# Optimization experiments

Hardware: AMD Instinct MI355X
Metric: run time of the kernel (lower is better)

The kernel has to match this reference:

```python
import jax, jax.numpy as jnp
import numpy as np

N_NODES = 20000
DIM = 128
N_EDGES = 500000
BATCH = 16384
EPS = 1e-6  # torch.nn.PairwiseDistance default eps


def setup_inputs() -> dict:
    key = jax.random.key(0)
    k = jax.random.split(key, 8)
    edges = jax.random.randint(k[0], (2, N_EDGES), 0, N_NODES, dtype=jnp.int64 if jax.config.jax_enable_x64 else jnp.int32)
    nodes_p_star = jnp.sort(jax.random.randint(k[1], (BATCH,), 0, N_NODES))
    nodes_p = jnp.sort(jax.random.randint(k[2], (BATCH,), 0, N_NODES))
    # learned parameters, init in [-1, 1) as in the torch module
    beta_p = 2.0 * jax.random.uniform(k[3], (N_NODES,), dtype=jnp.float32) - 1.0
    beta_p_star = 2.0 * jax.random.uniform(k[4], (N_NODES,), dtype=jnp.float32) - 1.0
    p = 2.0 * jax.random.uniform(k[5], (N_NODES, DIM), dtype=jnp.float32) - 1.0
    p_star = 2.0 * jax.random.uniform(k[6], (N_NODES, DIM), dtype=jnp.float32) - 1.0
    return {
        "edges": edges,
        "nodes_p_star": nodes_p_star,
        "nodes_p": nodes_p,
        "beta_p": beta_p,
        "beta_p_star": beta_p_star,
        "p": p,
        "p_star": p_star,
    }


def reference(edges, nodes_p_star, nodes_p, beta_p, beta_p_star, p, p_star):
    # ---- link term: sum over observed edges of (beta - dist) ----
    beta_pair = beta_p_star[edges[0]] + beta_p[edges[1]]  # [E]
    diff = p[edges[0]] - p_star[edges[1]]                 # [E, D]
    # torch PairwiseDistance adds eps to the difference before the norm
    z_dist = jnp.sqrt(jnp.sum((diff + EPS) ** 2, axis=-1))
    link_term = jnp.sum(beta_pair - z_dist)

    # ---- non-link term: triu-masked sum of exp(beta - cdist) ----
    bps = beta_p_star[nodes_p_star]   # [Ns]
    bp = beta_p[nodes_p]              # [Np]
    ps = p_star[nodes_p_star]         # [Ns, D]
    pp = p[nodes_p]                   # [Np, D]
    beta_mat = bps[None, :] + bp[:, None]          # [Np, Ns]
    # cdist(ps, pp) -> [Ns, Np] via Gram trick
    sq = (jnp.sum(ps * ps, axis=-1)[:, None]
          + jnp.sum(pp * pp, axis=-1)[None, :]
          - 2.0 * jnp.einsum('nd,md->nm', ps, pp))
    dist_mat = jnp.sqrt(jnp.maximum(sq, 0.0))      # [Ns, Np]
    intensity = jnp.exp(beta_mat.T - dist_mat)     # [Ns, Np]
    non_link = jnp.sum(jnp.triu(intensity, k=1))

    return -(link_term - non_link)
```

## Files before the change

### kernel.cpp

```cpp
#include <hip/hip_runtime.h>
#include <hip/hip_bf16.h>

#define N_NODES 20000
#define DIM 128
#define N_EDGES 500000
#define BATCH 16384
#define EPS 1e-6f
#define L2E 1.4426950408889634f

typedef _Float16 half8 __attribute__((ext_vector_type(8)));
typedef _Float16 half4_t __attribute__((ext_vector_type(4)));
typedef float f32x4 __attribute__((ext_vector_type(4)));

__device__ __forceinline__ float fast_sqrtf(float x) {
#if __has_builtin(__builtin_amdgcn_sqrtf)
    return __builtin_amdgcn_sqrtf(x);
#else
    return sqrtf(x);
#endif
}
__device__ __forceinline__ float fast_exp2f(float x) {
#if __has_builtin(__builtin_amdgcn_exp2f)
    return __builtin_amdgcn_exp2f(x);
#else
    return exp2f(x);
#endif
}

#define NB_TILE 16512
#define NB_LINKB 4128
#define NB_MAIN 20640
#define LINK_EPB 128
#define NB_FIN 128

#define OFF_PGEMM 0
#define OFF_PLINK 66048
#define OFF_FPART 82560
#define OFF_PSH   83072
#define OFF_PPH   4277376
#define OFF_N2S   8471680
#define OFF_N2P   8537216
#define OFF_BPS   8602752
#define OFF_BP    8668288
#define OFF_P16   8733824
#define OFF_PS16  13853824
#define OFF_END   18973824

__global__ __launch_bounds__(256) void prep_kernel(
    const float* __restrict__ p, const float* __restrict__ p_star,
    const float* __restrict__ beta_p, const float* __restrict__ beta_ps,
    const int* __restrict__ nodes_ps, const int* __restrict__ nodes_p,
    _Float16* __restrict__ Ah, float* __restrict__ n2A, float* __restrict__ bA2,
    _Float16* __restrict__ Bh, float* __restrict__ n2B, float* __restrict__ bB2,
    _Float16* __restrict__ p16, _Float16* __restrict__ ps16)
{
    const int bx = blockIdx.x;
    const int g = threadIdx.x & 31;
    const int r8 = threadIdx.x >> 5;
    if (bx < 4096) {
        const bool isA = bx < 2048;
        int row = (isA ? bx : bx - 2048) * 8 + r8;
        int id = isA ? nodes_ps[row] : nodes_p[row];
        const float* src = isA ? p_star : p;
        float4 v = ((const float4*)(src + (size_t)id * DIM))[g];
        half4_t o;
        o[0] = (_Float16)v.x; o[1] = (_Float16)v.y; o[2] = (_Float16)v.z; o[3] = (_Float16)v.w;
        _Float16* dst = isA ? Ah : Bh;
        *(half4_t*)(dst + (size_t)row * DIM + g * 4) = o;
        float nrm = v.x * v.x + v.y * v.y + v.z * v.z + v.w * v.w;
        #pragma unroll
        for (int m = 16; m >= 1; m >>= 1) nrm += __shfl_xor(nrm, m, 32);
        if (g == 0) {
            if (isA) { n2A[row] = nrm; bA2[row] = L2E * beta_ps[id]; }
            else     { n2B[row] = nrm; bB2[row] = L2E * beta_p[id]; }
        }
    } else {
        const bool isP = bx < 6596;
        int row = (isP ? bx - 4096 : bx - 6596) * 8 + r8;
        const float* src = isP ? p : p_star;
        _Float16* dst = isP ? p16 : ps16;
        float4 v = ((const float4*)(src + (size_t)row * DIM))[g];
        half4_t o;
        o[0] = (_Float16)v.x; o[1] = (_Float16)v.y; o[2] = (_Float16)v.z; o[3] = (_Float16)v.w;
        *(half4_t*)(dst + (size_t)row * DIM + g * 4) = o;
    }
}

__global__ __launch_bounds__(256) void main_kernel(
    const _Float16* __restrict__ Ag, const _Float16* __restrict__ Bg,
    const float* __restrict__ n2A, const float* __restrict__ n2B,
    const float* __restrict__ bA2, const float* __restrict__ bB2,
    const int* __restrict__ edges,
    const float* __restrict__ beta_p, const float* __restrict__ beta_ps,
    const _Float16* __restrict__ p16, const _Float16* __restrict__ ps16,
    const float* __restrict__ pf, const float* __restrict__ psf, int use16,
    float* __restrict__ pgemm, float* __restrict__ plink)
{
    const int f = blockIdx.x;
    const int grp5 = f / 5, rem5 = f % 5;
    const int tid = threadIdx.x;

    __shared__ __align__(16) _Float16 As[128][136];
    __shared__ __align__(16) _Float16 Bs[64][136];
    __shared__ float smr[4];

    if (rem5 == 4) {
        float tacc = 0.f;
        if (use16) {
            int g = tid & 15, grp = tid >> 4;
            #pragma unroll
            for (int t = 0; t < 8; ++t) {
                int e = grp5 * LINK_EPB + t * 16 + grp;
                if (e < N_EDGES) {
                    int e0 = edges[e];
                    int e1 = edges[N_EDGES + e];
                    half8 a = *(const half8*)(p16 + (size_t)e0 * DIM + g * 8);
                    half8 b = *(const half8*)(ps16 + (size_t)e1 * DIM + g * 8);
                    float s = 0.f;
                    #pragma unroll
                    for (int k = 0; k < 8; ++k) {
                        float d = (float)a[k] - (float)b[k] + EPS;
                        s = fmaf(d, d, s);
                    }
                    #pragma unroll
                    for (int m = 8; m >= 1; m >>= 1) s += __shfl_xor(s, m, 16);
                    if (g == 0) tacc += (beta_ps[e0] + beta_p[e1]) - fast_sqrtf(s);
                }
            }
        } else {
            int g = tid & 31, grp = tid >> 5;
            #pragma unroll
            for (int t = 0; t < 16; ++t) {
                int e = grp5 * LINK_EPB + t * 8 + grp;
                if (e < N_EDGES) {
                    int e0 = edges[e];
                    int e1 = edges[N_EDGES + e];
                    float4 a = ((const float4*)(pf + (size_t)e0 * DIM))[g];
                    float4 b = ((const float4*)(psf + (size_t)e1 * DIM))[g];
                    float dx = a.x - b.x + EPS, dy = a.y - b.y + EPS;
                    float dz = a.z - b.z + EPS, dw = a.w - b.w + EPS;
                    float s = dx * dx + dy * dy + dz * dz + dw * dw;
                    #pragma unroll
                    for (int m = 16; m >= 1; m >>= 1) s += __shfl_xor(s, m, 32);
                    if (g == 0) tacc += (beta_ps[e0] + beta_p[e1]) - fast_sqrtf(s);
                }
            }
        }
        #pragma unroll
        for (int m = 32; m >= 1; m >>= 1) tacc += __shfl_xor(tacc, m, 64);
        if ((tid & 63) == 0) smr[tid >> 6] = tacc;
        __syncthreads();
        if (tid == 0) plink[grp5] = smr[0] + smr[1] + smr[2] + smr[3];
        return;
    }

    const int t = grp5 * 4 + rem5;
    const int by = t / 258, bx = t % 258;
    int ti, tj;
    const int len = 256 - 2 * by;
    if (bx < len) { ti = by; tj = 2 * by + bx; }
    else          { ti = 127 - by; tj = bx - 2; }
    const int i0 = ti * 128;
    const int j0 = tj * 64;

    const int lane = tid & 63;
    const int w = tid >> 6;
    const int wm = w & 1;
    const int wn = w >> 1;
    const int quad = lane >> 4;
    const int lr = lane & 15;
    const int ilo = i0 + wm * 64;
    const int jlo = j0 + wn * 32;

    float4 n2i[4], bi[4];
    float n2j[2], bj[2];
    #pragma unroll
    for (int mi = 0; mi < 4; ++mi) {
        n2i[mi] = *(const float4*)&n2A[ilo + mi * 16 + quad * 4];
        bi[mi] = *(const float4*)&bA2[ilo + mi * 16 + quad * 4];
    }
    #pragma unroll
    for (int ni = 0; ni < 2; ++ni) {
        n2j[ni] = n2B[jlo + ni * 16 + lr];
        bj[ni] = bB2[jlo + ni * 16 + lr];
    }

    #pragma unroll
    for (int c = tid; c < 2048; c += 256)
        *(uint4*)&As[c >> 4][(c & 15) * 8] =
            *(const uint4*)(Ag + (size_t)(i0 + (c >> 4)) * DIM + (c & 15) * 8);
    #pragma unroll
    for (int c = tid; c < 1024; c += 256)
        *(uint4*)&Bs[c >> 4][(c & 15) * 8] =
            *(const uint4*)(Bg + (size_t)(j0 + (c >> 4)) * DIM + (c & 15) * 8);
    __syncthreads();

    const bool dead = (jlo + 31 <= ilo);
    const bool freew = (jlo > ilo + 63);

    float lsum = 0.f;
    if (!dead) {
        f32x4 acc[4][2] = {};
        #pragma unroll
        for (int ks = 0; ks < 4; ++ks) {
            int koff = ks * 32 + quad * 8;
            half8 af[4], bf[2];
            #pragma unroll
            for (int u = 0; u < 4; ++u) af[u] = *(const half8*)&As[wm * 64 + u * 16 + lr][koff];
            #pragma unroll
            for (int u = 0; u < 2; ++u) bf[u] = *(const half8*)&Bs[wn * 32 + u * 16 + lr][koff];
            #pragma unroll
            for (int mi = 0; mi < 4; ++mi)
                #pragma unroll
                for (int ni = 0; ni < 2; ++ni)
                    acc[mi][ni] = __builtin_amdgcn_mfma_f32_16x16x32_f16(af[mi], bf[ni], acc[mi][ni], 0, 0, 0);
        }

        if (freew) {
            #pragma unroll
            for (int mi = 0; mi < 4; ++mi)
                #pragma unroll
                for (int ni = 0; ni < 2; ++ni) {
                    f32x4 d = acc[mi][ni];
                    #pragma unroll
                    for (int r = 0; r < 4; ++r) {
                        float tt = ((const float*)&n2i[mi])[r] + n2j[ni];
                        float sq = fmaxf(fmaf(d[r], -2.f, tt), 0.f);
                        float dist = fast_sqrtf(sq);
                        float arg = fmaf(dist, -L2E, ((const float*)&bi[mi])[r] + bj[ni]);
                        lsum += fast_exp2f(arg);
                    }
                }
        } else {
            #pragma unroll
            for (int mi = 0; mi < 4; ++mi)
                #pragma unroll
                for (int ni = 0; ni < 2; ++ni) {
                    f32x4 d = acc[mi][ni];
                    #pragma unroll
                    for (int r = 0; r < 4; ++r) {
                        int ig = ilo + mi * 16 + quad * 4 + r;
                        int jg = jlo + ni * 16 + lr;
                        float tt = ((const float*)&n2i[mi])[r] + n2j[ni];
                        float sq = fmaxf(fmaf(d[r], -2.f, tt), 0.f);
                        float dist = fast_sqrtf(sq);
                        float arg = fmaf(dist, -L2E, ((const float*)&bi[mi])[r] + bj[ni]);
                        float ex = fast_exp2f(arg);
                        if (jg > ig) lsum += ex;
                    }
                }
        }
    }

    #pragma unroll
    for (int m = 32; m >= 1; m >>= 1) lsum += __shfl_xor(lsum, m, 64);
    if (lane == 0) smr[w] = lsum;
    __syncthreads();
    if (tid == 0) pgemm[t] = smr[0] + smr[1] + smr[2] + smr[3];
}

__global__ __launch_bounds__(256) void reduce1_kernel(
    const float* __restrict__ pg, const float* __restrict__ pl, float* __restrict__ fpart)
{
    float s = 0.f;
    for (int k = blockIdx.x * 256 + threadIdx.x; k < NB_TILE; k += NB_FIN * 256) s += pg[k];
    for (int k = blockIdx.x * 256 + threadIdx.x; k < NB_LINKB; k += NB_FIN * 256) s -= pl[k];
    #pragma unroll
    for (int m = 32; m >= 1; m >>= 1) s += __shfl_xor(s, m, 64);
    __shared__ float sm[4];
    int w = threadIdx.x >> 6;
    if ((threadIdx.x & 63) == 0) sm[w] = s;
    __syncthreads();
    if (threadIdx.x == 0) fpart[blockIdx.x] = sm[0] + sm[1] + sm[2] + sm[3];
}

__global__ __launch_bounds__(128) void reduce2_kernel(
    const float* __restrict__ fpart, float* __restrict__ out)
{
    float s = fpart[threadIdx.x];
    #pragma unroll
    for (int m = 32; m >= 1; m >>= 1) s += __shfl_xor(s, m, 64);
    __shared__ float sm[2];
    if ((threadIdx.x & 63) == 0) sm[threadIdx.x >> 6] = s;
    __syncthreads();
    if (threadIdx.x == 0) out[0] = sm[0] + sm[1];
}

extern "C" void kernel_launch(void* const* d_in, const int* in_sizes, int n_in,
                              void* d_out, int out_size, void* d_ws, size_t ws_size,
                              hipStream_t stream) {
    const int* edges = (const int*)d_in[0];
    const int* nodes_p_star = (const int*)d_in[1];
    const int* nodes_p = (const int*)d_in[2];
    const float* beta_p = (const float*)d_in[3];
    const float* beta_p_star = (const float*)d_in[4];
    const float* p = (const float*)d_in[5];
    const float* p_star = (const float*)d_in[6];

    char* ws = (char*)d_ws;
    float* pgemm = (float*)(ws + OFF_PGEMM);
    float* plink = (float*)(ws + OFF_PLINK);
    float* fpart = (float*)(ws + OFF_FPART);
    _Float16* psh = (_Float16*)(ws + OFF_PSH);
    _Float16* pph = (_Float16*)(ws + OFF_PPH);
    float* n2s = (float*)(ws + OFF_N2S);
    float* n2p = (float*)(ws + OFF_N2P);
    float* bps2 = (float*)(ws + OFF_BPS);
    float* bp2 = (float*)(ws + OFF_BP);
    _Float16* p16 = (_Float16*)(ws + OFF_P16);
    _Float16* ps16 = (_Float16*)(ws + OFF_PS16);

    const int use16 = (ws_size >= (size_t)OFF_END) ? 1 : 0;

    prep_kernel<<<9096, 256, 0, stream>>>(
        p, p_star, beta_p, beta_p_star, nodes_p_star, nodes_p,
        psh, n2s, bps2, pph, n2p, bp2, p16, ps16);

    main_kernel<<<NB_MAIN, 256, 0, stream>>>(
        psh, pph, n2s, n2p, bps2, bp2,
        edges, beta_p, beta_p_star, p16, ps16, p, p_star, use16,
        pgemm, plink);

    reduce1_kernel<<<NB_FIN, 256, 0, stream>>>(pgemm, plink, fpart);
    reduce2_kernel<<<1, 128, 0, stream>>>(fpart, (float*)d_out);
}
```

Baseline: 237.5 us.

## Use 128x128 triangular tiles with 512 threads and fuse link edges into GEMM blocks

Replaces the 128x64 tiles with 128x128 square tiles over the upper triangle, processed by 512-thread blocks on a 2D grid. Instead of dedicated link blocks, each tile block now gathers 64 edges up front and finishes their distances after the MFMA epilogue, so the gather latency overlaps the GEMM. The two-stage reduction becomes a single 1024-thread reduce kernel. The aim is to cut redundant row loads, block count and launch overhead, at the cost of more LDS per block and heavier per-block work.

```diff
diff --git a/kernel.cpp b/kernel.cpp
--- a/kernel.cpp
+++ b/kernel.cpp
@@ -27,24 +27,18 @@
 #endif
 }
 
-#define NB_TILE 16512
-#define NB_LINKB 4128
-#define NB_MAIN 20640
-#define LINK_EPB 128
-#define NB_FIN 128
+#define NB_TILE 8256
 
 #define OFF_PGEMM 0
-#define OFF_PLINK 66048
-#define OFF_FPART 82560
-#define OFF_PSH   83072
-#define OFF_PPH   4277376
-#define OFF_N2S   8471680
-#define OFF_N2P   8537216
-#define OFF_BPS   8602752
-#define OFF_BP    8668288
-#define OFF_P16   8733824
-#define OFF_PS16  13853824
-#define OFF_END   18973824
+#define OFF_PSH   33280
+#define OFF_PPH   4227584
+#define OFF_N2S   8421888
+#define OFF_N2P   8487424
+#define OFF_BPS   8552960
+#define OFF_BP    8618496
+#define OFF_P16   8684032
+#define OFF_PS16  13804032
+#define OFF_END   18924032
 
 __global__ __launch_bounds__(256) void prep_kernel(
     const float* __restrict__ p, const float* __restrict__ p_star,
@@ -86,7 +80,7 @@
     }
 }
 
-__global__ __launch_bounds__(256) void main_kernel(
+__global__ __launch_bounds__(512, 4) void main_kernel(
     const _Float16* __restrict__ Ag, const _Float16* __restrict__ Bg,
     const float* __restrict__ n2A, const float* __restrict__ n2B,
     const float* __restrict__ bA2, const float* __restrict__ bB2,
@@ -94,148 +88,123 @@
     const float* __restrict__ beta_p, const float* __restrict__ beta_ps,
     const _Float16* __restrict__ p16, const _Float16* __restrict__ ps16,
     const float* __restrict__ pf, const float* __restrict__ psf, int use16,
-    float* __restrict__ pgemm, float* __restrict__ plink)
+    float* __restrict__ pgemm)
 {
-    const int f = blockIdx.x;
-    const int grp5 = f / 5, rem5 = f % 5;
+    const int bx = blockIdx.x, by = blockIdx.y;
+    int ti, tj;
+    const int len = 128 - by;
+    if (bx < len) { ti = by; tj = by + bx; }
+    else          { ti = 127 - by; tj = 127 - (bx - len); }
+    const int i0 = ti * 128, j0 = tj * 128;
+    const int bid = by * 129 + bx;
+    const bool diag = (ti == tj);
+
+    __shared__ __align__(16) _Float16 As[128][136];
+    __shared__ __align__(16) _Float16 Bs[128][136];
+    __shared__ float smr[8];
+
     const int tid = threadIdx.x;
-
-    __shared__ __align__(16) _Float16 As[128][136];
-    __shared__ __align__(16) _Float16 Bs[64][136];
-    __shared__ float smr[4];
-
-    if (rem5 == 4) {
-        float tacc = 0.f;
-        if (use16) {
-            int g = tid & 15, grp = tid >> 4;
-            #pragma unroll
-            for (int t = 0; t < 8; ++t) {
-                int e = grp5 * LINK_EPB + t * 16 + grp;
-                if (e < N_EDGES) {
-                    int e0 = edges[e];
-                    int e1 = edges[N_EDGES + e];
-                    half8 a = *(const half8*)(p16 + (size_t)e0 * DIM + g * 8);
-                    half8 b = *(const half8*)(ps16 + (size_t)e1 * DIM + g * 8);
+    const int lane = tid & 63;
+    const int w = tid >> 6;
+    const int wm = w & 3;
+    const int wn = w >> 2;
+    const int quad = lane >> 4;
+    const int lr = lane & 15;
+
+    float lsum = 0.f;
+    half8 ea[2], eb[2];
+    float ebeta[2] = {0.f, 0.f};
+    bool ev[2];
+    {
+        #pragma unroll
+        for (int t = 0; t < 2; ++t) {
+            int e = bid * 64 + w * 8 + quad * 2 + t;
+            ev[t] = (e < N_EDGES);
+            if (ev[t]) {
+                int e0 = edges[e];
+                int e1 = edges[N_EDGES + e];
+                if (use16) {
+                    ea[t] = *(const half8*)(p16 + (size_t)e0 * DIM + lr * 8);
+                    eb[t] = *(const half8*)(ps16 + (size_t)e1 * DIM + lr * 8);
+                    if (lr == 0) ebeta[t] = beta_ps[e0] + beta_p[e1];
+                } else {
+                    const float* ar = pf + (size_t)e0 * DIM + lr * 8;
+                    const float* br = psf + (size_t)e1 * DIM + lr * 8;
                     float s = 0.f;
                     #pragma unroll
                     for (int k = 0; k < 8; ++k) {
-                        float d = (float)a[k] - (float)b[k] + EPS;
+                        float d = ar[k] - br[k] + EPS;
                         s = fmaf(d, d, s);
                     }
                     #pragma unroll
                     for (int m = 8; m >= 1; m >>= 1) s += __shfl_xor(s, m, 16);
-                    if (g == 0) tacc += (beta_ps[e0] + beta_p[e1]) - fast_sqrtf(s);
+                    if (lr == 0) lsum -= (beta_ps[e0] + beta_p[e1]) - fast_sqrtf(s);
                 }
             }
-        } else {
-            int g = tid & 31, grp = tid >> 5;
-            #pragma unroll
-            for (int t = 0; t < 16; ++t) {
-                int e = grp5 * LINK_EPB + t * 8 + grp;
-                if (e < N_EDGES) {
-                    int e0 = edges[e];
-                    int e1 = edges[N_EDGES + e];
-                    float4 a = ((const float4*)(pf + (size_t)e0 * DIM))[g];
-                    float4 b = ((const float4*)(psf + (size_t)e1 * DIM))[g];
-                    float dx = a.x - b.x + EPS, dy = a.y - b.y + EPS;
-                    float dz = a.z - b.z + EPS, dw = a.w - b.w + EPS;
-                    float s = dx * dx + dy * dy + dz * dz + dw * dw;
-                    #pragma unroll
-                    for (int m = 16; m >= 1; m >>= 1) s += __shfl_xor(s, m, 32);
-                    if (g == 0) tacc += (beta_ps[e0] + beta_p[e1]) - fast_sqrtf(s);
-                }
-            }
-        }
-        #pragma unroll
-        for (int m = 32; m >= 1; m >>= 1) tacc += __shfl_xor(tacc, m, 64);
-        if ((tid & 63) == 0) smr[tid >> 6] = tacc;
-        __syncthreads();
-        if (tid == 0) plink[grp5] = smr[0] + smr[1] + smr[2] + smr[3];
-        return;
-    }
-
-    const int t = grp5 * 4 + rem5;
-    const int by = t / 258, bx = t % 258;
-    int ti, tj;
-    const int len = 256 - 2 * by;
-    if (bx < len) { ti = by; tj = 2 * by + bx; }
-    else          { ti = 127 - by; tj = bx - 2; }
-    const int i0 = ti * 128;
-    const int j0 = tj * 64;
-
-    const int lane = tid & 63;
-    const int w = tid >> 6;
-    const int wm = w & 1;
-    const int wn = w >> 1;
-    const int quad = lane >> 4;
-    const int lr = lane & 15;
-    const int ilo = i0 + wm * 64;
-    const int jlo = j0 + wn * 32;
-
-    float4 n2i[4], bi[4];
-    float n2j[2], bj[2];
-    #pragma unroll
-    for (int mi = 0; mi < 4; ++mi) {
+        }
+    }
+
+    const int ilo = i0 + wm * 32, jlo = j0 + wn * 64;
+    float4 n2i[2], bi[2];
+    #pragma unroll
+    for (int mi = 0; mi < 2; ++mi) {
         n2i[mi] = *(const float4*)&n2A[ilo + mi * 16 + quad * 4];
-        bi[mi] = *(const float4*)&bA2[ilo + mi * 16 + quad * 4];
-    }
-    #pragma unroll
-    for (int ni = 0; ni < 2; ++ni) {
+        bi[mi]  = *(const float4*)&bA2[ilo + mi * 16 + quad * 4];
+    }
+    float n2j[4], bj[4];
+    #pragma unroll
+    for (int ni = 0; ni < 4; ++ni) {
         n2j[ni] = n2B[jlo + ni * 16 + lr];
-        bj[ni] = bB2[jlo + ni * 16 + lr];
-    }
-
-    #pragma unroll
-    for (int c = tid; c < 2048; c += 256)
-        *(uint4*)&As[c >> 4][(c & 15) * 8] =
-            *(const uint4*)(Ag + (size_t)(i0 + (c >> 4)) * DIM + (c & 15) * 8);
-    #pragma unroll
-    for (int c = tid; c < 1024; c += 256)
-        *(uint4*)&Bs[c >> 4][(c & 15) * 8] =
-            *(const uint4*)(Bg + (size_t)(j0 + (c >> 4)) * DIM + (c & 15) * 8);
+        bj[ni]  = bB2[jlo + ni * 16 + lr];
+    }
+
+    #pragma unroll
+    for (int c = tid; c < 2048; c += 512) {
+        int row = c >> 4, col = (c & 15) * 8;
+        *(uint4*)&As[row][col] = *(const uint4*)(Ag + (size_t)(i0 + row) * DIM + col);
+        *(uint4*)&Bs[row][col] = *(const uint4*)(Bg + (size_t)(j0 + row) * DIM + col);
+    }
     __syncthreads();
 
-    const bool dead = (jlo + 31 <= ilo);
-    const bool freew = (jlo > ilo + 63);
-
-    float lsum = 0.f;
-    if (!dead) {
-        f32x4 acc[4][2] = {};
+    int cls = 0;
+    if (diag) cls = (wn == 0) ? (wm >= 2 ? 2 : 1) : (wm >= 2 ? 1 : 0);
+
+    if (cls != 2) {
+        f32x4 acc[2][4] = {};
         #pragma unroll
         for (int ks = 0; ks < 4; ++ks) {
             int koff = ks * 32 + quad * 8;
-            half8 af[4], bf[2];
-            #pragma unroll
-            for (int u = 0; u < 4; ++u) af[u] = *(const half8*)&As[wm * 64 + u * 16 + lr][koff];
-            #pragma unroll
-            for (int u = 0; u < 2; ++u) bf[u] = *(const half8*)&Bs[wn * 32 + u * 16 + lr][koff];
-            #pragma unroll
-            for (int mi = 0; mi < 4; ++mi)
-                #pragma unroll
-                for (int ni = 0; ni < 2; ++ni)
+            half8 af[2], bf[4];
+            #pragma unroll
+            for (int u = 0; u < 2; ++u) af[u] = *(const half8*)&As[wm * 32 + u * 16 + lr][koff];
+            #pragma unroll
+            for (int v = 0; v < 4; ++v) bf[v] = *(const half8*)&Bs[wn * 64 + v * 16 + lr][koff];
+            #pragma unroll
+            for (int mi = 0; mi < 2; ++mi)
+                #pragma unroll
+                for (int ni = 0; ni < 4; ++ni)
                     acc[mi][ni] = __builtin_amdgcn_mfma_f32_16x16x32_f16(af[mi], bf[ni], acc[mi][ni], 0, 0, 0);
         }
 
-        if (freew) {
-            #pragma unroll
-            for (int mi = 0; mi < 4; ++mi)
-                #pragma unroll
-                for (int ni = 0; ni < 2; ++ni) {
+        if (cls == 0) {
+            #pragma unroll
+            for (int mi = 0; mi < 2; ++mi)
+                #pragma unroll
+                for (int ni = 0; ni < 4; ++ni) {
                     f32x4 d = acc[mi][ni];
                     #pragma unroll
                     for (int r = 0; r < 4; ++r) {
                         float tt = ((const float*)&n2i[mi])[r] + n2j[ni];
                         float sq = fmaxf(fmaf(d[r], -2.f, tt), 0.f);
-                        float dist = fast_sqrtf(sq);
-                        float arg = fmaf(dist, -L2E, ((const float*)&bi[mi])[r] + bj[ni]);
+                        float arg = fmaf(fast_sqrtf(sq), -L2E, ((const float*)&bi[mi])[r] + bj[ni]);
                         lsum += fast_exp2f(arg);
                     }
                 }
         } else {
             #pragma unroll
-            for (int mi = 0; mi < 4; ++mi)
-                #pragma unroll
-                for (int ni = 0; ni < 2; ++ni) {
+            for (int mi = 0; mi < 2; ++mi)
+                #pragma unroll
+                for (int ni = 0; ni < 4; ++ni) {
                     f32x4 d = acc[mi][ni];
                     #pragma unroll
                     for (int r = 0; r < 4; ++r) {
@@ -243,8 +212,7 @@
                         int jg = jlo + ni * 16 + lr;
                         float tt = ((const float*)&n2i[mi])[r] + n2j[ni];
                         float sq = fmaxf(fmaf(d[r], -2.f, tt), 0.f);
-                        float dist = fast_sqrtf(sq);
-                        float arg = fmaf(dist, -L2E, ((const float*)&bi[mi])[r] + bj[ni]);
+                        float arg = fmaf(fast_sqrtf(sq), -L2E, ((const float*)&bi[mi])[r] + bj[ni]);
                         float ex = fast_exp2f(arg);
                         if (jg > ig) lsum += ex;
                     }
@@ -252,38 +220,51 @@
         }
     }
 
+    if (use16) {
+        #pragma unroll
+        for (int t = 0; t < 2; ++t) {
+            if (ev[t]) {
+                float s = 0.f;
+                #pragma unroll
+                for (int k = 0; k < 8; ++k) {
+                    float d = (float)ea[t][k] - (float)eb[t][k] + EPS;
+                    s = fmaf(d, d, s);
+                }
+                #pragma unroll
+                for (int m = 8; m >= 1; m >>= 1) s += __shfl_xor(s, m, 16);
+                if (lr == 0) lsum -= ebeta[t] - fast_sqrtf(s);
+            }
+        }
+    }
+
     #pragma unroll
     for (int m = 32; m >= 1; m >>= 1) lsum += __shfl_xor(lsum, m, 64);
     if (lane == 0) smr[w] = lsum;
     __syncthreads();
-    if (tid == 0) pgemm[t] = smr[0] + smr[1] + smr[2] + smr[3];
-}
-
-__global__ __launch_bounds__(256) void reduce1_kernel(
-    const float* __restrict__ pg, const float* __restrict__ pl, float* __restrict__ fpart)
+    if (tid == 0) {
+        float t = 0.f;
+        #pragma unroll
+        for (int i = 0; i < 8; ++i) t += smr[i];
+        pgemm[bid] = t;
+    }
+}
+
+__global__ __launch_bounds__(1024) void reduce_kernel(
+    const float* __restrict__ pg, float* __restrict__ out)
 {
     float s = 0.f;
-    for (int k = blockIdx.x * 256 + threadIdx.x; k < NB_TILE; k += NB_FIN * 256) s += pg[k];
-    for (int k = blockIdx.x * 256 + threadIdx.x; k < NB_LINKB; k += NB_FIN * 256) s -= pl[k];
+    for (int k = threadIdx.x; k < NB_TILE; k += 1024) s += pg[k];
     #pragma unroll
     for (int m = 32; m >= 1; m >>= 1) s += __shfl_xor(s, m, 64);
-    __shared__ float sm[4];
-    int w = threadIdx.x >> 6;
-    if ((threadIdx.x & 63) == 0) sm[w] = s;
-    __syncthreads();
-    if (threadIdx.x == 0) fpart[blockIdx.x] = sm[0] + sm[1] + sm[2] + sm[3];
-}
-
-__global__ __launch_bounds__(128) void reduce2_kernel(
-    const float* __restrict__ fpart, float* __restrict__ out)
-{
-    float s = fpart[threadIdx.x];
-    #pragma unroll
-    for (int m = 32; m >= 1; m >>= 1) s += __shfl_xor(s, m, 64);
-    __shared__ float sm[2];
+    __shared__ float sm[16];
     if ((threadIdx.x & 63) == 0) sm[threadIdx.x >> 6] = s;
     __syncthreads();
-    if (threadIdx.x == 0) out[0] = sm[0] + sm[1];
+    if (threadIdx.x == 0) {
+        float t = 0.f;
+        #pragma unroll
+        for (int i = 0; i < 16; ++i) t += sm[i];
+        out[0] = t;
+    }
 }
 
 extern "C" void kernel_launch(void* const* d_in, const int* in_sizes, int n_in,
@@ -299,8 +280,6 @@
 
     char* ws = (char*)d_ws;
     float* pgemm = (float*)(ws + OFF_PGEMM);
-    float* plink = (float*)(ws + OFF_PLINK);
-    float* fpart = (float*)(ws + OFF_FPART);
     _Float16* psh = (_Float16*)(ws + OFF_PSH);
     _Float16* pph = (_Float16*)(ws + OFF_PPH);
     float* n2s = (float*)(ws + OFF_N2S);
@@ -316,11 +295,10 @@
         p, p_star, beta_p, beta_p_star, nodes_p_star, nodes_p,
         psh, n2s, bps2, pph, n2p, bp2, p16, ps16);
 
-    main_kernel<<<NB_MAIN, 256, 0, stream>>>(
+    main_kernel<<<dim3(129, 64), 512, 0, stream>>>(
         psh, pph, n2s, n2p, bps2, bp2,
         edges, beta_p, beta_p_star, p16, ps16, p, p_star, use16,
-        pgemm, plink);
-
-    reduce1_kernel<<<NB_FIN, 256, 0, stream>>>(pgemm, plink, fpart);
-    reduce2_kernel<<<1, 128, 0, stream>>>(fpart, (float*)d_out);
-}
+        pgemm);
+
+    reduce_kernel<<<1, 1024, 0, stream>>>(pgemm, (float*)d_out);
+}
```

Result: faster. 193.4 us (-18.5%).
